# Optimization experiments

Measured on AMD Instinct MI355X. Metric: run time of the kernel, lower is better.

The kernel has to match this reference:

```python
import jax, jax.numpy as jnp
import numpy as np

EMBED_DIM = 256
NUM_HEADS = 8
NUM_LEVELS = 4
NUM_POINTS = 4
HEAD_DIM = EMBED_DIM // NUM_HEADS


def _bilinear_sample(img, x, y):
    """img: [N,C,H,W]; x,y: [N,P] absolute pixel coords (align_corners=False mapping
    already applied by caller). Zero padding outside, matching F.grid_sample."""
    N, C, H, W = img.shape
    x0 = jnp.floor(x)
    y0 = jnp.floor(y)
    wx1 = x - x0
    wy1 = y - y0
    img_flat = img.reshape(N, C, H * W)

    def gather(ix, iy):
        valid = ((ix >= 0) & (ix <= W - 1) & (iy >= 0) & (iy <= H - 1)).astype(img.dtype)
        idx = (jnp.clip(iy, 0, H - 1) * W + jnp.clip(ix, 0, W - 1)).astype(jnp.int32)
        v = jnp.take_along_axis(img_flat, idx[:, None, :], axis=2)  # [N,C,P]
        return v * valid[:, None, :]

    return (gather(x0, y0) * ((1.0 - wx1) * (1.0 - wy1))[:, None, :]
            + gather(x0 + 1.0, y0) * (wx1 * (1.0 - wy1))[:, None, :]
            + gather(x0, y0 + 1.0) * ((1.0 - wx1) * wy1)[:, None, :]
            + gather(x0 + 1.0, y0 + 1.0) * (wx1 * wy1)[:, None, :])


def _reference_points(H, W):
    yy, xx = jnp.meshgrid(jnp.arange(H, dtype=jnp.float32), jnp.arange(W, dtype=jnp.float32), indexing='ij')
    # stack order is (x, y), matching grid_sample's (x=width, y=height) convention
    return jnp.stack([(xx + 0.5) / W, (yy + 0.5) / H], axis=-1).reshape(H * W, 2)


def _frame_attention(q_feat, values, level_shapes, Wq, bq, Woff, boff, Wattn, battn, Wout, bout):
    Bt, C, H, W = q_feat.shape
    N = H * W
    q = q_feat.reshape(Bt, C, N).transpose(0, 2, 1) @ Wq + bq  # [Bt,N,C]
    off = (q @ Woff + boff).reshape(Bt, N, NUM_HEADS, NUM_LEVELS, NUM_POINTS, 2)
    aw = jax.nn.softmax((q @ Wattn + battn).reshape(Bt, N, NUM_HEADS, NUM_LEVELS * NUM_POINTS), axis=-1)
    aw = aw.reshape(Bt, N, NUM_HEADS, NUM_LEVELS, NUM_POINTS)
    ref = _reference_points(H, W)  # [N,2]
    sampled = []
    for l, (val, (Hl, Wl)) in enumerate(zip(values, level_shapes)):
        loc = ref[None, :, None, None, :] + off[:, :, :, l] / jnp.array([Wl, Hl], dtype=q.dtype)
        grid = jnp.clip(loc, 0.0, 1.0) * 2.0 - 1.0  # [Bt,N,M,K,2]
        grid = grid.transpose(0, 2, 1, 3, 4).reshape(Bt * NUM_HEADS, N * NUM_POINTS, 2)
        # align_corners=False: pixel = ((g+1)*size - 1)/2
        x = ((grid[..., 0] + 1.0) * Wl - 1.0) * 0.5
        y = ((grid[..., 1] + 1.0) * Hl - 1.0) * 0.5
        s = _bilinear_sample(val, x, y)  # [Bt*M, hd, N*K]
        s = s.reshape(Bt, NUM_HEADS, HEAD_DIM, N, NUM_POINTS).transpose(0, 3, 1, 4, 2)  # [Bt,N,M,K,hd]
        sampled.append(s)
    samp = jnp.stack(sampled, axis=3)  # [Bt,N,M,L,K,hd]
    out = (samp * aw[..., None]).sum(axis=(3, 4)).reshape(Bt, N, C)
    out = out @ Wout + bout
    return out.transpose(0, 2, 1).reshape(Bt, C, H, W)


def _forward(feats, Wq, bq, Wv, bv, Woff, boff, Wattn, battn, Wout, bout):
    B, C, H0, W0, T = feats[0].shape
    # original loops over frames t; frames are independent, so fold T into batch
    feats_bt = [jnp.moveaxis(f, -1, 1).reshape(f.shape[0] * T, C, f.shape[2], f.shape[3]) for f in feats]
    level_shapes = [(f.shape[2], f.shape[3]) for f in feats_bt]
    Bt = B * T
    # value projection per level (identical across query scales; compute once)
    values = []
    for f, (Hl, Wl) in zip(feats_bt, level_shapes):
        v = f.reshape(Bt, C, Hl * Wl).transpose(0, 2, 1) @ Wv + bv  # [Bt,HW,C]
        v = v.reshape(Bt, Hl * Wl, NUM_HEADS, HEAD_DIM).transpose(0, 2, 3, 1).reshape(Bt * NUM_HEADS, HEAD_DIM, Hl, Wl)
        values.append(v)
    outs = []
    for f, (Hl, Wl) in zip(feats_bt, level_shapes):
        o = _frame_attention(f, values, level_shapes, Wq, bq, Woff, boff, Wattn, battn, Wout, bout)
        outs.append(o.reshape(B, T, C, Hl, Wl).transpose(0, 2, 3, 4, 1))  # back to [B,C,H,W,T]
    return tuple(outs)


def setup_inputs() -> dict:
    key = jax.random.key(0)
    ks = jax.random.split(key, 10)
    B, T, C = 2, 2, EMBED_DIM
    shapes = [(64, 64), (32, 32), (16, 16), (8, 8)]
    inp = {}
    for i, (H, W) in enumerate(shapes):
        inp[f"feats{i}"] = jax.random.normal(ks[i], (B, C, H, W, T), dtype=jnp.float32)
    s = float(1.0 / np.sqrt(C))
    noff = NUM_HEADS * NUM_LEVELS * NUM_POINTS
    inp["Wq"] = jax.random.normal(ks[4], (C, C), jnp.float32) * s
    inp["bq"] = jnp.zeros((C,), jnp.float32)
    inp["Wv"] = jax.random.normal(ks[5], (C, C), jnp.float32) * s
    inp["bv"] = jnp.zeros((C,), jnp.float32)
    inp["Woff"] = jax.random.normal(ks[6], (C, noff * 2), jnp.float32) * 0.01
    inp["boff"] = jax.random.normal(ks[7], (noff * 2,), jnp.float32) * 2.0
    inp["Wattn"] = jax.random.normal(ks[8], (C, noff), jnp.float32) * 0.01
    inp["battn"] = jnp.zeros((noff,), jnp.float32)
    inp["Wout"] = jax.random.normal(ks[9], (C, C), jnp.float32) * s
    inp["bout"] = jnp.zeros((C,), jnp.float32)
    return inp


def reference(feats0, feats1, feats2, feats3, Wq, bq, Wv, bv, Woff, boff, Wattn, battn, Wout, bout):
    return _forward([feats0, feats1, feats2, feats3], Wq, bq, Wv, bv, Woff, boff, Wattn, battn, Wout, bout)
```

## Files before the change

### kernel.cpp

```cpp
#include <hip/hip_runtime.h>
#include <hip/hip_bf16.h>

#define NR 21760

typedef short short8 __attribute__((ext_vector_type(8)));
typedef float f32x4 __attribute__((ext_vector_type(4)));

__device__ __forceinline__ int level_of_row(int R) {
    if (R < 16384) return 0;
    if (R < 20480) return 1;
    if (R < 21504) return 2;
    return 3;
}

__device__ __forceinline__ unsigned pk2(float a, float b) {
    __hip_bfloat16 x = __float2bfloat16(a), y = __float2bfloat16(b);
    return (unsigned)*(unsigned short*)&x | ((unsigned)*(unsigned short*)&y << 16);
}

__global__ __launch_bounds__(256) void pack_all_kernel(const float* __restrict__ f0,
                                                       const float* __restrict__ f1,
                                                       const float* __restrict__ f2,
                                                       const float* __restrict__ f3,
                                                       __hip_bfloat16* __restrict__ XP) {
    int bx = blockIdx.x;
    const float* f; int nj, Wl, rowbase, rel;
    if (bx < 1024)      { f = f0; nj = 128; Wl = 64; rowbase = 0;     rel = bx; }
    else if (bx < 1280) { f = f1; nj = 32;  Wl = 32; rowbase = 16384; rel = bx - 1024; }
    else if (bx < 1344) { f = f2; nj = 8;   Wl = 16; rowbase = 20480; rel = bx - 1280; }
    else                { f = f3; nj = 2;   Wl = 8;  rowbase = 21504; rel = bx - 1344; }
    const int HW = Wl * Wl;
    const int HWT = HW * 2;
    const int j0 = (rel % nj) * 64;
    const int c0 = ((rel / nj) & 3) * 64;
    const int b  = rel / (nj * 4);
    __shared__ float tile[64][65];
    {
        const int tj = threadIdx.x & 63;
        const int tcb = threadIdx.x >> 6;
        const float* fb = f + (size_t)(b * 256 + c0) * HWT + j0;
#pragma unroll
        for (int i = 0; i < 16; ++i) {
            int cl = tcb + i * 4;
            tile[cl][tj] = fb[(size_t)cl * HWT + tj];
        }
    }
    __syncthreads();
    {
        const int tc = threadIdx.x & 63;
        const int tjb = threadIdx.x >> 6;
#pragma unroll
        for (int i = 0; i < 16; ++i) {
            int jl = tjb + i * 4;
            int j = j0 + jl;
            int p = j >> 1, t = j & 1;
            int row = rowbase + (b * 2 + t) * HW + p;
            XP[(size_t)row * 256 + c0 + tc] = __float2bfloat16(tile[tc][jl]);
        }
    }
}

__global__ __launch_bounds__(256) void wtrans_all_kernel(const float* __restrict__ Wq,
                                                         const float* __restrict__ Wv,
                                                         const float* __restrict__ Woff,
                                                         const float* __restrict__ Wattn,
                                                         const float* __restrict__ Wout,
                                                         const float* __restrict__ bq,
                                                         const float* __restrict__ boff,
                                                         const float* __restrict__ battn,
                                                         __hip_bfloat16* __restrict__ WTv,
                                                         __hip_bfloat16* __restrict__ WToa,
                                                         __hip_bfloat16* __restrict__ Wqb,
                                                         __hip_bfloat16* __restrict__ WTout,
                                                         float* __restrict__ bias_oa) {
    const int bx = blockIdx.x;
    const int tid = threadIdx.x;
    if (bx == 256) {
        {
            int n = tid;
            float s = 0.f;
            for (int j = 0; j < 256; ++j) s += bq[j] * Woff[(size_t)j * 256 + n];
            bias_oa[n] = s + boff[n];
        }
        if (tid < 128) {
            int n = tid;
            float s = 0.f;
            for (int j = 0; j < 256; ++j) s += bq[j] * Wattn[(size_t)j * 128 + n];
            bias_oa[256 + n] = s + battn[n];
        }
        return;
    }
    if (bx >= 160 && bx < 192) {
        int e0 = (bx - 160) * 2048 + tid * 8;
        float4 a = *(const float4*)(Wq + e0);
        float4 b = *(const float4*)(Wq + e0 + 4);
        uint4 o;
        o.x = pk2(a.x, a.y); o.y = pk2(a.z, a.w);
        o.z = pk2(b.x, b.y); o.w = pk2(b.z, b.w);
        *(uint4*)(&Wqb[e0]) = o;
        return;
    }
    __shared__ float t[32][33];
    const float* W; __hip_bfloat16* WT; int N; int rel;
    if (bx < 64)       { W = Wv;    WT = WTv;              N = 256; rel = bx; }
    else if (bx < 128) { W = Woff;  WT = WToa;             N = 256; rel = bx - 64; }
    else if (bx < 160) { W = Wattn; WT = WToa + 256 * 256; N = 128; rel = bx - 128; }
    else               { W = Wout;  WT = WTout;            N = 256; rel = bx - 192; }
    const int K = 256;
    const int ntiles = N >> 5;
    const int n0 = (rel % ntiles) * 32, k0 = (rel / ntiles) * 32;
    const int c = tid & 31, r = tid >> 5;
#pragma unroll
    for (int i = 0; i < 4; ++i)
        t[r + 8 * i][c] = W[(size_t)(k0 + r + 8 * i) * N + n0 + c];
    __syncthreads();
#pragma unroll
    for (int i = 0; i < 4; ++i)
        WT[(size_t)(n0 + r + 8 * i) * K + k0 + c] = __float2bfloat16(t[c][r + 8 * i]);
}

template <int OUTMODE>
__global__ __launch_bounds__(256) void gemm_mfma(const __hip_bfloat16* __restrict__ A,
                                                 const __hip_bfloat16* __restrict__ BT,
                                                 const float* __restrict__ bias,
                                                 void* __restrict__ Cout,
                                                 int M, int N, int K) {
    __shared__ __align__(16) __hip_bfloat16 As[64][72];
    __shared__ __align__(16) __hip_bfloat16 Bs[64][72];
    const int m0 = blockIdx.x * 64;
    const int n0 = blockIdx.y * 64;
    const int w = threadIdx.x >> 6;
    const int lane = threadIdx.x & 63;
    const int wm = (w >> 1) * 32;
    const int wn = (w & 1) * 32;
    const int fr = lane & 15;
    const int fq = lane >> 4;
    const int srow = threadIdx.x >> 3;
    const int schunk = threadIdx.x & 7;
    f32x4 acc[2][2] = {};

    for (int kt = 0; kt < K; kt += 64) {
        __syncthreads();
#pragma unroll
        for (int i = 0; i < 2; ++i) {
            int r = srow + 32 * i;
            float4 va = *(const float4*)(&A[(size_t)(m0 + r) * K + kt + schunk * 8]);
            *(float4*)(&As[r][schunk * 8]) = va;
            float4 vb = *(const float4*)(&BT[(size_t)(n0 + r) * K + kt + schunk * 8]);
            *(float4*)(&Bs[r][schunk * 8]) = vb;
        }
        __syncthreads();
#pragma unroll
        for (int ks = 0; ks < 2; ++ks) {
            short8 a[2], b[2];
#pragma unroll
            for (int fi = 0; fi < 2; ++fi)
                a[fi] = *(const short8*)(&As[wm + fi * 16 + fr][ks * 32 + fq * 8]);
#pragma unroll
            for (int fj = 0; fj < 2; ++fj)
                b[fj] = *(const short8*)(&Bs[wn + fj * 16 + fr][ks * 32 + fq * 8]);
#pragma unroll
            for (int fi = 0; fi < 2; ++fi)
#pragma unroll
                for (int fj = 0; fj < 2; ++fj)
                    acc[fi][fj] = __builtin_amdgcn_mfma_f32_16x16x32_bf16(
                        a[fi], b[fj], acc[fi][fj], 0, 0, 0);
        }
    }

    if (OUTMODE == 2) {
        const int lvl = level_of_row(m0);
        const int qbase[4]   = {0, 16384, 20480, 21504};
        const int wtab[4]    = {64, 32, 16, 8};
        const size_t obase[4] = {0, 4194304, 5242880, 5505024};
        const int Wl = wtab[lvl];
        const int HW = Wl * Wl;
        float* out = (float*)Cout;
#pragma unroll
        for (int fi = 0; fi < 2; ++fi)
#pragma unroll
            for (int fj = 0; fj < 2; ++fj) {
                int col = n0 + wn + fj * 16 + fr;
                float bb = bias[col];
#pragma unroll
                for (int r = 0; r < 4; ++r) {
                    int row = m0 + wm + fi * 16 + fq * 4 + r;
                    int r2 = row - qbase[lvl];
                    int bt = r2 / HW;
                    int p  = r2 - bt * HW;
                    int b  = bt >> 1, t = bt & 1;
                    int y  = p / Wl, x = p - y * Wl;
                    size_t addr = obase[lvl] +
                        ((((size_t)b * 256 + col) * Wl + y) * Wl + x) * 2 + t;
                    out[addr] = acc[fi][fj][r] + bb;
                }
            }
    } else {
#pragma unroll
        for (int fi = 0; fi < 2; ++fi)
#pragma unroll
            for (int fj = 0; fj < 2; ++fj) {
                int col = n0 + wn + fj * 16 + fr;
                float bb = bias ? bias[col] : 0.f;
#pragma unroll
                for (int r = 0; r < 4; ++r) {
                    int row = m0 + wm + fi * 16 + fq * 4 + r;
                    float v = acc[fi][fj][r] + bb;
                    if (OUTMODE == 0)
                        ((float*)Cout)[(size_t)row * N + col] = v;
                    else
                        ((__hip_bfloat16*)Cout)[(size_t)row * N + col] = __float2bfloat16(v);
                }
            }
    }
}

__device__ __forceinline__ void acc8(f32x4& a, f32x4& b, uint4 v, float w) {
    a[0] = fmaf(w, __uint_as_float(v.x << 16),          a[0]);
    a[1] = fmaf(w, __uint_as_float(v.x & 0xffff0000u),  a[1]);
    a[2] = fmaf(w, __uint_as_float(v.y << 16),          a[2]);
    a[3] = fmaf(w, __uint_as_float(v.y & 0xffff0000u),  a[3]);
    b[0] = fmaf(w, __uint_as_float(v.z << 16),          b[0]);
    b[1] = fmaf(w, __uint_as_float(v.z & 0xffff0000u),  b[1]);
    b[2] = fmaf(w, __uint_as_float(v.w << 16),          b[2]);
    b[3] = fmaf(w, __uint_as_float(v.w & 0xffff0000u),  b[3]);
}

#define QB 4
__global__ __launch_bounds__(256, 2) void sample_kernel(const __hip_bfloat16* __restrict__ VAL,
                                                        const float* __restrict__ OA,
                                                        __hip_bfloat16* __restrict__ SAMP) {
    __shared__ __align__(16) int2 tapd[QB * 512];
    const int R0 = blockIdx.x * QB;
    const int tid = threadIdx.x;
    const int qbase[4] = {0, 16384, 20480, 21504};
    const int wsh[4]   = {6, 5, 4, 3};
    const int hwsh[4]  = {12, 10, 8, 6};
    const float invwf[4] = {1.f/64.f, 1.f/32.f, 1.f/16.f, 1.f/8.f};

    if (tid < QB * 32) {
        const int qh = tid >> 2, part = tid & 3;
        const int q = qh >> 3, h = qh & 7;
        const int R = R0 + q;
        const int lq = level_of_row(R);
        const int r2 = R - qbase[lq];
        const int bt = r2 >> hwsh[lq];
        const int p  = r2 & ((1 << hwsh[lq]) - 1);
        const int pxi = p & ((1 << wsh[lq]) - 1);
        const int pyi = p >> wsh[lq];
        const float refx = (pxi + 0.5f) * invwf[lq];
        const float refy = (pyi + 0.5f) * invwf[lq];
        const float* oarow = OA + (size_t)R * 384;
        float4 offA = *(const float4*)(oarow + h * 32 + part * 8);
        float4 offB = *(const float4*)(oarow + h * 32 + part * 8 + 4);
        float4 awv  = *(const float4*)(oarow + 256 + h * 16 + part * 4);
        float m = fmaxf(fmaxf(awv.x, awv.y), fmaxf(awv.z, awv.w));
        m = fmaxf(m, __shfl_xor(m, 1));
        m = fmaxf(m, __shfl_xor(m, 2));
        float e0 = __expf(awv.x - m), e1 = __expf(awv.y - m);
        float e2 = __expf(awv.z - m), e3 = __expf(awv.w - m);
        float s = e0 + e1 + e2 + e3;
        s += __shfl_xor(s, 1);
        s += __shfl_xor(s, 2);
        const float inv = 1.0f / s;
        const int l = part;
        const int Wl = 1 << wsh[l];
        const float invWf = invwf[l];
        const int base = (qbase[l] + (bt << hwsh[l])) << 8;
        float oxy[8] = {offA.x, offA.y, offA.z, offA.w, offB.x, offB.y, offB.z, offB.w};
        float ee[4] = {e0, e1, e2, e3};
#pragma unroll
        for (int i = 0; i < 4; ++i) {
            float ox = oxy[2 * i], oy = oxy[2 * i + 1];
            float aw = ee[i] * inv;
            float lx = fminf(fmaxf(refx + ox * invWf, 0.f), 1.f);
            float ly = fminf(fmaxf(refy + oy * invWf, 0.f), 1.f);
            float px = lx * Wl - 0.5f;
            float py = ly * Wl - 0.5f;
            float x0f = floorf(px), y0f = floorf(py);
            int x0 = (int)x0f, y0 = (int)y0f;
            float wx = px - x0f, wy = py - y0f;
            float vx0 = (x0 >= 0) ? 1.f : 0.f;
            float vx1 = (x0 + 1 <= Wl - 1) ? 1.f : 0.f;
            float vy0 = (y0 >= 0) ? 1.f : 0.f;
            float vy1 = (y0 + 1 <= Wl - 1) ? 1.f : 0.f;
            int x0c = max(x0, 0), x1c = min(x0 + 1, Wl - 1);
            int y0c = max(y0, 0), y1c = min(y0 + 1, Wl - 1);
            int o00 = base + (((y0c << wsh[l]) + x0c) << 8);
            int o10 = base + (((y0c << wsh[l]) + x1c) << 8);
            int o01 = base + (((y1c << wsh[l]) + x0c) << 8);
            int o11 = base + (((y1c << wsh[l]) + x1c) << 8);
            float w00 = aw * (1.f - wx) * (1.f - wy) * vx0 * vy0;
            float w10 = aw * wx * (1.f - wy) * vx1 * vy0;
            float w01 = aw * (1.f - wx) * wy * vx0 * vy1;
            float w11 = aw * wx * wy * vx1 * vy1;
            int idx = ((q * 16 + part * 4 + i) * 8 + h) * 4;
            *(int4*)(&tapd[idx])     = make_int4(o00, __float_as_int(w00), o10, __float_as_int(w10));
            *(int4*)(&tapd[idx + 2]) = make_int4(o01, __float_as_int(w01), o11, __float_as_int(w11));
        }
    }
    __syncthreads();

    const int wq = tid >> 6, lane = tid & 63;
    const int u = lane >> 2, sub = lane & 3;
    const int c = u & 3, h4 = u >> 2;
    const int R = R0 + wq;
    const __hip_bfloat16* v0base = VAL + h4 * 32 + sub * 8;
    const __hip_bfloat16* v1base = VAL + (h4 + 4) * 32 + sub * 8;
    const int2* tp = &tapd[wq * 512];
    f32x4 aA0 = {0,0,0,0}, aA1 = {0,0,0,0};
    f32x4 aB0 = {0,0,0,0}, aB1 = {0,0,0,0};
#pragma unroll 2
    for (int t = 0; t < 16; ++t) {
        int2 d0 = tp[(t * 8 + h4) * 4 + c];
        int2 d1 = tp[(t * 8 + h4 + 4) * 4 + c];
        uint4 x0 = *(const uint4*)(v0base + d0.x);
        uint4 x1 = *(const uint4*)(v1base + d1.x);
        acc8(aA0, aA1, x0, __int_as_float(d0.y));
        acc8(aB0, aB1, x1, __int_as_float(d1.y));
    }
#pragma unroll
    for (int i = 0; i < 4; ++i) {
        aA0[i] += __shfl_xor(aA0[i], 4); aA0[i] += __shfl_xor(aA0[i], 8);
        aA1[i] += __shfl_xor(aA1[i], 4); aA1[i] += __shfl_xor(aA1[i], 8);
        aB0[i] += __shfl_xor(aB0[i], 4); aB0[i] += __shfl_xor(aB0[i], 8);
        aB1[i] += __shfl_xor(aB1[i], 4); aB1[i] += __shfl_xor(aB1[i], 8);
    }
    if (c == 0) {
        uint4 o0, o1;
        o0.x = pk2(aA0[0], aA0[1]); o0.y = pk2(aA0[2], aA0[3]);
        o0.z = pk2(aA1[0], aA1[1]); o0.w = pk2(aA1[2], aA1[3]);
        o1.x = pk2(aB0[0], aB0[1]); o1.y = pk2(aB0[2], aB0[3]);
        o1.z = pk2(aB1[0], aB1[1]); o1.w = pk2(aB1[2], aB1[3]);
        *(uint4*)(&SAMP[(size_t)R * 256 + h4 * 32 + sub * 8]) = o0;
        *(uint4*)(&SAMP[(size_t)R * 256 + (h4 + 4) * 32 + sub * 8]) = o1;
    }
}

extern "C" void kernel_launch(void* const* d_in, const int* in_sizes, int n_in,
                              void* d_out, int out_size, void* d_ws, size_t ws_size,
                              hipStream_t stream) {
    (void)in_sizes; (void)n_in; (void)out_size; (void)ws_size;
    const float* f0 = (const float*)d_in[0];
    const float* f1 = (const float*)d_in[1];
    const float* f2 = (const float*)d_in[2];
    const float* f3 = (const float*)d_in[3];
    const float* Wq    = (const float*)d_in[4];
    const float* bq    = (const float*)d_in[5];
    const float* Wv    = (const float*)d_in[6];
    const float* bv    = (const float*)d_in[7];
    const float* Woff  = (const float*)d_in[8];
    const float* boff  = (const float*)d_in[9];
    const float* Wattn = (const float*)d_in[10];
    const float* battn = (const float*)d_in[11];
    const float* Wout  = (const float*)d_in[12];
    const float* bout  = (const float*)d_in[13];
    float* out = (float*)d_out;

    char* w = (char*)d_ws;
    __hip_bfloat16* XPb   = (__hip_bfloat16*)w;   w += (size_t)NR * 256 * 2;
    __hip_bfloat16* SAMPb = (__hip_bfloat16*)w;   w += (size_t)NR * 256 * 2;
    __hip_bfloat16* VAL   = (__hip_bfloat16*)w;   w += (size_t)NR * 256 * 2;
    float* OA   = (float*)w;                      w += (size_t)NR * 384 * 4;
    __hip_bfloat16* WTv   = (__hip_bfloat16*)w;   w += 256 * 256 * 2;
    __hip_bfloat16* WToa  = (__hip_bfloat16*)w;   w += 384 * 256 * 2;
    __hip_bfloat16* Wqb   = (__hip_bfloat16*)w;   w += 256 * 256 * 2;
    __hip_bfloat16* WpT   = (__hip_bfloat16*)w;   w += 384 * 256 * 2;
    __hip_bfloat16* WTout = (__hip_bfloat16*)w;   w += 256 * 256 * 2;
    float* bias_oa = (float*)w;                   w += 384 * 4;

    hipLaunchKernelGGL(pack_all_kernel, dim3(1360), dim3(256), 0, stream, f0, f1, f2, f3, XPb);

    hipLaunchKernelGGL(wtrans_all_kernel, dim3(257), dim3(256), 0, stream,
                       Wq, Wv, Woff, Wattn, Wout, bq, boff, battn,
                       WTv, WToa, Wqb, WTout, bias_oa);

    hipLaunchKernelGGL((gemm_mfma<3>), dim3(6, 4), dim3(256), 0, stream,
                       WToa, Wqb, nullptr, (void*)WpT, 384, 256, 256);

    hipLaunchKernelGGL((gemm_mfma<3>), dim3(NR / 64, 4), dim3(256), 0, stream,
                       XPb, WTv, bv, (void*)VAL, NR, 256, 256);

    hipLaunchKernelGGL((gemm_mfma<0>), dim3(NR / 64, 6), dim3(256), 0, stream,
                       XPb, WpT, bias_oa, (void*)OA, NR, 384, 256);

    hipLaunchKernelGGL(sample_kernel, dim3(NR / QB), dim3(256), 0, stream, VAL, OA, SAMPb);

    hipLaunchKernelGGL((gemm_mfma<2>), dim3(NR / 64, 4), dim3(256), 0, stream,
                       SAMPb, WTout, bout, (void*)out, NR, 256, 256);
}
```

Measured before the change: 119.9 us.

## Fuse value and offset GEMMs, vectorize pack, and coalesce output scatter

Merges the value projection and the offset/attention projection into one GEMM over a concatenated 640-column weight, so the input is read once and one launch is removed. The pack kernel now uses float4 loads and packed bf16 stores. The output projection becomes a dedicated kernel that remaps rows so both time steps land in adjacent lanes, letting it write float2 pairs into the [B,C,H,W,T] layout instead of scattered scalar stores. The sample kernel's block order is also swizzled across levels for better load balance. The cost is extra code paths with hand-computed index maps that must match the level layout exactly.

```diff
diff --git a/kernel.cpp b/kernel.cpp
--- a/kernel.cpp
+++ b/kernel.cpp
@@ -34,28 +34,33 @@
     const int j0 = (rel % nj) * 64;
     const int c0 = ((rel / nj) & 3) * 64;
     const int b  = rel / (nj * 4);
+    const int tid = threadIdx.x;
     __shared__ float tile[64][65];
     {
-        const int tj = threadIdx.x & 63;
-        const int tcb = threadIdx.x >> 6;
-        const float* fb = f + (size_t)(b * 256 + c0) * HWT + j0;
-#pragma unroll
-        for (int i = 0; i < 16; ++i) {
-            int cl = tcb + i * 4;
-            tile[cl][tj] = fb[(size_t)cl * HWT + tj];
+        const int cl = tid >> 2, q = tid & 3;
+        const float* fb = f + (size_t)(b * 256 + c0 + cl) * HWT + j0 + q * 16;
+#pragma unroll
+        for (int k = 0; k < 4; ++k) {
+            float4 v = *(const float4*)(fb + k * 4);
+            *(float4*)(&tile[cl][q * 16 + k * 4]) = v;
         }
     }
     __syncthreads();
     {
-        const int tc = threadIdx.x & 63;
-        const int tjb = threadIdx.x >> 6;
-#pragma unroll
-        for (int i = 0; i < 16; ++i) {
-            int jl = tjb + i * 4;
-            int j = j0 + jl;
+        const int jl = tid >> 4, cq = tid & 15;
+#pragma unroll
+        for (int pass = 0; pass < 4; ++pass) {
+            int jloc = pass * 16 + jl;
+            int j = j0 + jloc;
             int p = j >> 1, t = j & 1;
             int row = rowbase + (b * 2 + t) * HW + p;
-            XP[(size_t)row * 256 + c0 + tc] = __float2bfloat16(tile[tc][jl]);
+            float v0 = tile[cq * 4 + 0][jloc];
+            float v1 = tile[cq * 4 + 1][jloc];
+            float v2 = tile[cq * 4 + 2][jloc];
+            float v3 = tile[cq * 4 + 3][jloc];
+            uint2 o;
+            o.x = pk2(v0, v1); o.y = pk2(v2, v3);
+            *(uint2*)(&XP[(size_t)row * 256 + c0 + cq * 4]) = o;
         }
     }
 }
@@ -68,7 +73,7 @@
                                                          const float* __restrict__ bq,
                                                          const float* __restrict__ boff,
                                                          const float* __restrict__ battn,
-                                                         __hip_bfloat16* __restrict__ WTv,
+                                                         __hip_bfloat16* __restrict__ WTvo,
                                                          __hip_bfloat16* __restrict__ WToa,
                                                          __hip_bfloat16* __restrict__ Wqb,
                                                          __hip_bfloat16* __restrict__ WTout,
@@ -102,7 +107,7 @@
     }
     __shared__ float t[32][33];
     const float* W; __hip_bfloat16* WT; int N; int rel;
-    if (bx < 64)       { W = Wv;    WT = WTv;              N = 256; rel = bx; }
+    if (bx < 64)       { W = Wv;    WT = WTvo;             N = 256; rel = bx; }
     else if (bx < 128) { W = Woff;  WT = WToa;             N = 256; rel = bx - 64; }
     else if (bx < 160) { W = Wattn; WT = WToa + 256 * 256; N = 128; rel = bx - 128; }
     else               { W = Wout;  WT = WTout;            N = 256; rel = bx - 192; }
@@ -123,7 +128,9 @@
 __global__ __launch_bounds__(256) void gemm_mfma(const __hip_bfloat16* __restrict__ A,
                                                  const __hip_bfloat16* __restrict__ BT,
                                                  const float* __restrict__ bias,
+                                                 const float* __restrict__ bias2,
                                                  void* __restrict__ Cout,
+                                                 void* __restrict__ Cout2,
                                                  int M, int N, int K) {
     __shared__ __align__(16) __hip_bfloat16 As[64][72];
     __shared__ __align__(16) __hip_bfloat16 Bs[64][72];
@@ -168,33 +175,36 @@
         }
     }
 
-    if (OUTMODE == 2) {
-        const int lvl = level_of_row(m0);
-        const int qbase[4]   = {0, 16384, 20480, 21504};
-        const int wtab[4]    = {64, 32, 16, 8};
-        const size_t obase[4] = {0, 4194304, 5242880, 5505024};
-        const int Wl = wtab[lvl];
-        const int HW = Wl * Wl;
-        float* out = (float*)Cout;
-#pragma unroll
-        for (int fi = 0; fi < 2; ++fi)
-#pragma unroll
-            for (int fj = 0; fj < 2; ++fj) {
-                int col = n0 + wn + fj * 16 + fr;
-                float bb = bias[col];
-#pragma unroll
-                for (int r = 0; r < 4; ++r) {
-                    int row = m0 + wm + fi * 16 + fq * 4 + r;
-                    int r2 = row - qbase[lvl];
-                    int bt = r2 / HW;
-                    int p  = r2 - bt * HW;
-                    int b  = bt >> 1, t = bt & 1;
-                    int y  = p / Wl, x = p - y * Wl;
-                    size_t addr = obase[lvl] +
-                        ((((size_t)b * 256 + col) * Wl + y) * Wl + x) * 2 + t;
-                    out[addr] = acc[fi][fj][r] + bb;
+    if (OUTMODE == 4) {
+        if (n0 < 256) {
+            __hip_bfloat16* dst = (__hip_bfloat16*)Cout;
+#pragma unroll
+            for (int fi = 0; fi < 2; ++fi)
+#pragma unroll
+                for (int fj = 0; fj < 2; ++fj) {
+                    int col = n0 + wn + fj * 16 + fr;
+                    float bb = bias[col];
+#pragma unroll
+                    for (int r = 0; r < 4; ++r) {
+                        int row = m0 + wm + fi * 16 + fq * 4 + r;
+                        dst[(size_t)row * 256 + col] = __float2bfloat16(acc[fi][fj][r] + bb);
+                    }
                 }
-            }
+        } else {
+            float* dst = (float*)Cout2;
+#pragma unroll
+            for (int fi = 0; fi < 2; ++fi)
+#pragma unroll
+                for (int fj = 0; fj < 2; ++fj) {
+                    int col = n0 - 256 + wn + fj * 16 + fr;
+                    float bb = bias2[col];
+#pragma unroll
+                    for (int r = 0; r < 4; ++r) {
+                        int row = m0 + wm + fi * 16 + fq * 4 + r;
+                        dst[(size_t)row * 384 + col] = acc[fi][fj][r] + bb;
+                    }
+                }
+        }
     } else {
 #pragma unroll
         for (int fi = 0; fi < 2; ++fi)
@@ -205,13 +215,87 @@
 #pragma unroll
                 for (int r = 0; r < 4; ++r) {
                     int row = m0 + wm + fi * 16 + fq * 4 + r;
-                    float v = acc[fi][fj][r] + bb;
-                    if (OUTMODE == 0)
-                        ((float*)Cout)[(size_t)row * N + col] = v;
-                    else
-                        ((__hip_bfloat16*)Cout)[(size_t)row * N + col] = __float2bfloat16(v);
+                    ((__hip_bfloat16*)Cout)[(size_t)row * N + col] =
+                        __float2bfloat16(acc[fi][fj][r] + bb);
                 }
             }
+    }
+}
+
+__global__ __launch_bounds__(256) void gemm_scatter_kernel(const __hip_bfloat16* __restrict__ A,
+                                                           const __hip_bfloat16* __restrict__ BT,
+                                                           const float* __restrict__ bias,
+                                                           float* __restrict__ out) {
+    const int bx = blockIdx.x;
+    int l, b, p0;
+    if (bx < 256)      { l = 0; b = bx >> 7;          p0 = (bx & 127) * 32; }
+    else if (bx < 320) { l = 1; b = (bx - 256) >> 5;  p0 = ((bx - 256) & 31) * 32; }
+    else if (bx < 336) { l = 2; b = (bx - 320) >> 3;  p0 = ((bx - 320) & 7) * 32; }
+    else               { l = 3; b = (bx - 336) >> 1;  p0 = ((bx - 336) & 1) * 32; }
+    const int qbase[4]    = {0, 16384, 20480, 21504};
+    const int hwtab[4]    = {4096, 1024, 256, 64};
+    const size_t obase[4] = {0, 4194304, 5242880, 5505024};
+    const int HW = hwtab[l];
+    const int qb = qbase[l];
+
+    __shared__ __align__(16) __hip_bfloat16 As[64][72];
+    __shared__ __align__(16) __hip_bfloat16 Bs[64][72];
+    const int n0 = blockIdx.y * 64;
+    const int w = threadIdx.x >> 6;
+    const int lane = threadIdx.x & 63;
+    const int wm = (w >> 1) * 32;
+    const int wn = (w & 1) * 32;
+    const int fr = lane & 15;
+    const int fq = lane >> 4;
+    const int srow = threadIdx.x >> 3;
+    const int schunk = threadIdx.x & 7;
+    f32x4 acc[2][2] = {};
+
+    for (int kt = 0; kt < 256; kt += 64) {
+        __syncthreads();
+#pragma unroll
+        for (int i = 0; i < 2; ++i) {
+            int m = srow + 32 * i;
+            int t = (m >> 4) & 1;
+            int pl = (m & 15) | ((m & 32) >> 1);
+            int R = qb + (2 * b + t) * HW + p0 + pl;
+            float4 va = *(const float4*)(&A[(size_t)R * 256 + kt + schunk * 8]);
+            *(float4*)(&As[m][schunk * 8]) = va;
+            float4 vb = *(const float4*)(&BT[(size_t)(n0 + m) * 256 + kt + schunk * 8]);
+            *(float4*)(&Bs[m][schunk * 8]) = vb;
+        }
+        __syncthreads();
+#pragma unroll
+        for (int ks = 0; ks < 2; ++ks) {
+            short8 a[2], bfr[2];
+#pragma unroll
+            for (int fi = 0; fi < 2; ++fi)
+                a[fi] = *(const short8*)(&As[wm + fi * 16 + fr][ks * 32 + fq * 8]);
+#pragma unroll
+            for (int fj = 0; fj < 2; ++fj)
+                bfr[fj] = *(const short8*)(&Bs[wn + fj * 16 + fr][ks * 32 + fq * 8]);
+#pragma unroll
+            for (int fi = 0; fi < 2; ++fi)
+#pragma unroll
+                for (int fj = 0; fj < 2; ++fj)
+                    acc[fi][fj] = __builtin_amdgcn_mfma_f32_16x16x32_bf16(
+                        a[fi], bfr[fj], acc[fi][fj], 0, 0, 0);
+        }
+    }
+    const int plbase = fq * 4 + ((wm & 32) >> 1);
+#pragma unroll
+    for (int fj = 0; fj < 2; ++fj) {
+        int col = n0 + wn + fj * 16 + fr;
+        float bb = bias[col];
+#pragma unroll
+        for (int r = 0; r < 4; ++r) {
+            int p = p0 + plbase + r;
+            size_t addr = obase[l] + (((size_t)b * 256 + col) * HW + p) * 2;
+            float2 v;
+            v.x = acc[0][fj][r] + bb;
+            v.y = acc[1][fj][r] + bb;
+            *(float2*)(out + addr) = v;
+        }
     }
 }
 
@@ -231,7 +315,9 @@
                                                         const float* __restrict__ OA,
                                                         __hip_bfloat16* __restrict__ SAMP) {
     __shared__ __align__(16) int2 tapd[QB * 512];
-    const int R0 = blockIdx.x * QB;
+    const int blk = blockIdx.x;
+    const int work = (blk & 7) * 680 + (blk >> 3);
+    const int R0 = work * QB;
     const int tid = threadIdx.x;
     const int qbase[4] = {0, 16384, 20480, 21504};
     const int wsh[4]   = {6, 5, 4, 3};
@@ -362,10 +448,9 @@
     __hip_bfloat16* SAMPb = (__hip_bfloat16*)w;   w += (size_t)NR * 256 * 2;
     __hip_bfloat16* VAL   = (__hip_bfloat16*)w;   w += (size_t)NR * 256 * 2;
     float* OA   = (float*)w;                      w += (size_t)NR * 384 * 4;
-    __hip_bfloat16* WTv   = (__hip_bfloat16*)w;   w += 256 * 256 * 2;
+    __hip_bfloat16* WTvo  = (__hip_bfloat16*)w;   w += 640 * 256 * 2;
     __hip_bfloat16* WToa  = (__hip_bfloat16*)w;   w += 384 * 256 * 2;
     __hip_bfloat16* Wqb   = (__hip_bfloat16*)w;   w += 256 * 256 * 2;
-    __hip_bfloat16* WpT   = (__hip_bfloat16*)w;   w += 384 * 256 * 2;
     __hip_bfloat16* WTout = (__hip_bfloat16*)w;   w += 256 * 256 * 2;
     float* bias_oa = (float*)w;                   w += 384 * 4;
 
@@ -373,19 +458,17 @@
 
     hipLaunchKernelGGL(wtrans_all_kernel, dim3(257), dim3(256), 0, stream,
                        Wq, Wv, Woff, Wattn, Wout, bq, boff, battn,
-                       WTv, WToa, Wqb, WTout, bias_oa);
+                       WTvo, WToa, Wqb, WTout, bias_oa);
 
     hipLaunchKernelGGL((gemm_mfma<3>), dim3(6, 4), dim3(256), 0, stream,
-                       WToa, Wqb, nullptr, (void*)WpT, 384, 256, 256);
-
-    hipLaunchKernelGGL((gemm_mfma<3>), dim3(NR / 64, 4), dim3(256), 0, stream,
-                       XPb, WTv, bv, (void*)VAL, NR, 256, 256);
-
-    hipLaunchKernelGGL((gemm_mfma<0>), dim3(NR / 64, 6), dim3(256), 0, stream,
-                       XPb, WpT, bias_oa, (void*)OA, NR, 384, 256);
+                       WToa, Wqb, nullptr, nullptr, (void*)(WTvo + 256 * 256), nullptr,
+                       384, 256, 256);
+
+    hipLaunchKernelGGL((gemm_mfma<4>), dim3(NR / 64, 10), dim3(256), 0, stream,
+                       XPb, WTvo, bv, bias_oa, (void*)VAL, (void*)OA, NR, 640, 256);
 
     hipLaunchKernelGGL(sample_kernel, dim3(NR / QB), dim3(256), 0, stream, VAL, OA, SAMPb);
 
-    hipLaunchKernelGGL((gemm_mfma<2>), dim3(NR / 64, 4), dim3(256), 0, stream,
-                       SAMPb, WTout, bout, (void*)out, NR, 256, 256);
-}
+    hipLaunchKernelGGL(gemm_scatter_kernel, dim3(340, 4), dim3(256), 0, stream,
+                       SAMPb, WTout, bout, out);
+}
```

Measured after the change: 105.3 us. -12.2%, faster.
